# Optimization experiments

Hardware: AMD Instinct MI355X
Metric: run time of the kernel (lower is better)

The kernel has to match this reference:

```python
import jax, jax.numpy as jnp
import numpy as np

N = 100000        # nodes
E = 1600000       # edges (avg degree 16)
IN_DIM = 256      # = H * OUT_DIM so residual is active
OUT_DIM = 32
H = 8             # heads
EPS = 1e-5        # BatchNorm eps


def setup_inputs() -> dict:
    key = jax.random.key(0)
    k1, k2, k3, k4, k5 = jax.random.split(key, 5)
    h = jax.random.normal(k1, (N, IN_DIM), jnp.float32)
    # per-head Linear(in_dim, out_dim, bias=False) weights, stacked: [H, O, D]
    W = jax.random.normal(k2, (H, OUT_DIM, IN_DIM), jnp.float32) / np.sqrt(IN_DIM)
    gamma = jnp.ones((H, OUT_DIM), jnp.float32)   # BN weight per head
    beta = jnp.zeros((H, OUT_DIM), jnp.float32)   # BN bias per head
    src = jax.random.randint(k3, (E,), 0, N, jnp.int32)
    dst = jax.random.randint(k4, (E,), 0, N, jnp.int32)
    e = jax.random.normal(k5, (E, 1), jnp.float32)  # edge feats: passthrough only
    return {"h": h, "W": W, "gamma": gamma, "beta": beta,
            "src": src, "dst": dst, "e": e}


def reference(h, W, gamma, beta, src, dst, e):
    # Per-head linear projection (all heads at once): z[n,h,o]
    z = jnp.einsum('nd,hod->nho', h, W)                    # [N, H, O]
    # message_func: copy src node 'z' along edges; reduce_func: sum over in-edges
    msg = z[src]                                           # [E, H, O] gather
    agg = jax.ops.segment_sum(msg, dst, num_segments=N)    # [N, H, O] scatter-add
    # BatchNorm1d per head (training-mode batch statistics, biased variance)
    mean = jnp.mean(agg, axis=0)                           # [H, O]
    var = jnp.var(agg, axis=0)                             # [H, O]
    hn = (agg - mean) * jax.lax.rsqrt(var + EPS) * gamma + beta
    hn = jax.nn.elu(hn)
    # dropout p=0.0 / eval mode -> identity
    out = hn.reshape(N, H * OUT_DIM)                       # concat heads
    # residual (in_dim == out_dim*num_heads)
    return h + out
```

## Files before the change

### kernel.cpp

```cpp
#include <hip/hip_runtime.h>
#include <hip/hip_bf16.h>

#define NCH 256
#define DIM 256
#define BN  64
#define NBMAX 2048
#define SEG 8
#define SEG2 2
#define ECHUNK 8192
#define SCAP 4096
#define NPART 64

using f32x4  = __attribute__((ext_vector_type(4))) float;
using s16x8  = __attribute__((ext_vector_type(8))) short;
using u16x8  = __attribute__((ext_vector_type(8))) unsigned short;

__device__ __forceinline__ unsigned short f2bf(float x) {
    unsigned u = __float_as_uint(x);
    u += 0x7FFFu + ((u >> 16) & 1u);
    return (unsigned short)(u >> 16);
}
__device__ __forceinline__ float bf2f(unsigned short b) {
    return __uint_as_float(((unsigned)b) << 16);
}

__device__ __forceinline__ int block_scan256_excl(int v, int* wtmp) {
    int lane = threadIdx.x & 63, wv = threadIdx.x >> 6;
    int x = v;
#pragma unroll
    for (int d = 1; d < 64; d <<= 1) {
        int t = __shfl_up(x, d);
        if (lane >= d) x += t;
    }
    if (lane == 63) wtmp[wv] = x;
    __syncthreads();
    int wbase = 0;
#pragma unroll
    for (int w = 0; w < 4; ++w) wbase += (w < wv) ? wtmp[w] : 0;
    __syncthreads();
    return wbase + x - v;
}

__device__ __forceinline__ int block_scan1024_excl(int v, int* wtmp) {
    int lane = threadIdx.x & 63, wv = threadIdx.x >> 6;
    int x = v;
#pragma unroll
    for (int d = 1; d < 64; d <<= 1) {
        int t = __shfl_up(x, d);
        if (lane >= d) x += t;
    }
    if (lane == 63) wtmp[wv] = x;
    __syncthreads();
    int wbase = 0;
#pragma unroll
    for (int w = 0; w < 16; ++w) wbase += (w < wv) ? wtmp[w] : 0;
    __syncthreads();
    return wbase + x - v;
}

__global__ __launch_bounds__(256) void cast_w_kernel(const float* __restrict__ W,
                                                     unsigned short* __restrict__ Wb) {
    int i = blockIdx.x * 256 + threadIdx.x;
    Wb[i] = f2bf(W[i]);
}

__global__ __launch_bounds__(512, 4) void gemm_z_kernel(const float* __restrict__ h,
                                                        const unsigned short* __restrict__ Wb,
                                                        unsigned short* __restrict__ z,
                                                        int N, int ntiles) {
    __shared__ __align__(16) unsigned short lds[32768];
    int by = blockIdx.y;

    const unsigned short* wsrc = Wb + (size_t)by * 32768;
    for (int it = 0; it < 8; ++it) {
        int c = it * 512 + threadIdx.x;
        int lin = c * 16;
        int dst = lin ^ (((lin >> 9) & 7) << 4);
        *reinterpret_cast<u16x8*>((char*)lds + dst) =
            *reinterpret_cast<const u16x8*>(wsrc + c * 8);
    }
    __syncthreads();

    int wv = threadIdx.x >> 6, lane = threadIdx.x & 63;
    int lrow = lane & 15;
    int lk   = (lane >> 4) * 8;

    int ldsoff[8];
#pragma unroll
    for (int kk = 0; kk < 8; ++kk)
        ldsoff[kk] = ((lrow * 512 + kk * 64 + lk * 2) ^ ((lrow & 7) << 4));

    for (int tile = blockIdx.x; tile < ntiles; tile += gridDim.x) {
        int r0 = tile * 128 + wv * 16;
        if (r0 >= N) continue;
        int row = r0 + lrow;

        float4 cur[16];
        if (row < N) {
            const float* ap = h + (size_t)row * DIM;
#pragma unroll
            for (int kk = 0; kk < 8; ++kk) {
                cur[2 * kk]     = *reinterpret_cast<const float4*>(ap + kk * 32 + lk);
                cur[2 * kk + 1] = *reinterpret_cast<const float4*>(ap + kk * 32 + lk + 4);
            }
        } else {
#pragma unroll
            for (int i = 0; i < 16; ++i) cur[i] = float4{0.f, 0.f, 0.f, 0.f};
        }

        f32x4 acc[8];
#pragma unroll
        for (int ct = 0; ct < 8; ++ct) acc[ct] = f32x4{0.f, 0.f, 0.f, 0.f};
#pragma unroll
        for (int kk = 0; kk < 8; ++kk) {
            union { s16x8 v; __hip_bfloat162 b2[4]; } u;
            float4 f0 = cur[2 * kk], f1 = cur[2 * kk + 1];
            u.b2[0] = __float22bfloat162_rn(float2{f0.x, f0.y});
            u.b2[1] = __float22bfloat162_rn(float2{f0.z, f0.w});
            u.b2[2] = __float22bfloat162_rn(float2{f1.x, f1.y});
            u.b2[3] = __float22bfloat162_rn(float2{f1.z, f1.w});
            s16x8 a = u.v;
#pragma unroll
            for (int ct = 0; ct < 8; ++ct) {
                s16x8 b = *reinterpret_cast<const s16x8*>(
                    (const char*)lds + (ldsoff[kk] + ct * 8192));
                acc[ct] = __builtin_amdgcn_mfma_f32_16x16x32_bf16(a, b, acc[ct], 0, 0, 0);
            }
        }
        int drow = (lane >> 4) * 4;
#pragma unroll
        for (int ct = 0; ct < 8; ++ct) {
#pragma unroll
            for (int r = 0; r < 4; ++r) {
                int orow = r0 + drow + r;
                if (orow < N)
                    z[(size_t)orow * NCH + by * 128 + ct * 16 + lrow] = f2bf(acc[ct][r]);
            }
        }
    }
}

__global__ __launch_bounds__(256) void bhist_kernel(const int* __restrict__ dst,
                                                    int* __restrict__ counts, int E, int NB) {
    __shared__ int cnt[NBMAX];
    int tid = threadIdx.x;
    for (int i = tid; i < NB; i += 256) cnt[i] = 0;
    __syncthreads();
    for (int j = blockIdx.x * 256 + tid; j < E; j += gridDim.x * 256)
        atomicAdd(&cnt[dst[j] >> 6], 1);
    __syncthreads();
    for (int i = tid; i < NB; i += 256)
        if (cnt[i]) atomicAdd(&counts[i], cnt[i]);
}

__global__ __launch_bounds__(256) void bscan_kernel(const int* __restrict__ counts,
                                                    int* __restrict__ bases,
                                                    int* __restrict__ cursor, int NB) {
    __shared__ int wtmp[4];
    int tid = threadIdx.x;
    int i0 = tid * SEG;
    int tsum = 0;
#pragma unroll
    for (int k = 0; k < SEG; ++k) {
        int idx = i0 + k;
        if (idx < NB) tsum += counts[idx];
    }
    int run = block_scan256_excl(tsum, wtmp);
#pragma unroll
    for (int k = 0; k < SEG; ++k) {
        int idx = i0 + k;
        if (idx < NB) {
            bases[idx]  = run;
            cursor[idx] = run;
            run += counts[idx];
        } else if (idx == NB) {
            bases[NB] = run;
        }
    }
}

__global__ __launch_bounds__(1024) void scatter1_kernel(const int* __restrict__ src,
                                                        const int* __restrict__ dst,
                                                        int* __restrict__ cursor,
                                                        unsigned* __restrict__ pairs,
                                                        int E, int NB) {
    __shared__ int cnt[NBMAX];
    __shared__ int excl0[NBMAX];
    __shared__ int gb[NBMAX];
    __shared__ unsigned staged[ECHUNK];
    __shared__ unsigned short sbkt[ECHUNK];
    __shared__ int wtmp[16];
    int tid = threadIdx.x;
    int base = blockIdx.x * ECHUNK;
    int n = min(ECHUNK, E - base);

    for (int i = tid; i < NB; i += 1024) cnt[i] = 0;
    __syncthreads();
    for (int j = tid; j < n; j += 1024)
        atomicAdd(&cnt[dst[base + j] >> 6], 1);
    __syncthreads();

    int i0 = tid * SEG2;
    int tsum = 0;
#pragma unroll
    for (int k = 0; k < SEG2; ++k) {
        int idx = i0 + k;
        if (idx < NB) tsum += cnt[idx];
    }
    int run = block_scan1024_excl(tsum, wtmp);
#pragma unroll
    for (int k = 0; k < SEG2; ++k) {
        int idx = i0 + k;
        if (idx < NB) {
            int c = cnt[idx];
            excl0[idx] = run;
            gb[idx] = c ? atomicAdd(&cursor[idx], c) : 0;
            run += c;
        }
    }
    __syncthreads();
    for (int i = tid; i < NB; i += 1024) cnt[i] = excl0[i];
    __syncthreads();
    for (int j = tid; j < n; j += 1024) {
        int d = dst[base + j];
        int b = d >> 6;
        int slot = atomicAdd(&cnt[b], 1);
        staged[slot] = (unsigned)src[base + j] | ((unsigned)(d & 63) << 17);
        sbkt[slot]   = (unsigned short)b;
    }
    __syncthreads();
    for (int j = tid; j < n; j += 1024) {
        int b = sbkt[j];
        pairs[gb[b] + (j - excl0[b])] = staged[j];
    }
}

__global__ __launch_bounds__(256) void sortb_kernel(unsigned* __restrict__ pairs,
                                                    const int* __restrict__ bases,
                                                    int* __restrict__ rowptr,
                                                    int N, int NB, int E) {
    __shared__ unsigned raw[SCAP];
    __shared__ unsigned srt[SCAP];
    __shared__ int cnt[BN];
    __shared__ int rp[BN + 1];
    __shared__ int cur[BN];
    int bkt = blockIdx.x, tid = threadIdx.x;
    int ebeg = bases[bkt];
    int ne = min(bases[bkt + 1] - ebeg, SCAP);

    if (tid < BN) cnt[tid] = 0;
    __syncthreads();
    for (int i = tid; i < ne; i += 256) {
        unsigned e = pairs[ebeg + i];
        raw[i] = e;
        atomicAdd(&cnt[(e >> 17) & 63], 1);
    }
    __syncthreads();
    if (tid < 64) {
        int x = cnt[tid];
#pragma unroll
        for (int d = 1; d < 64; d <<= 1) {
            int t = __shfl_up(x, d);
            if (tid >= d) x += t;
        }
        rp[tid + 1] = x;
        if (tid == 0) rp[0] = 0;
    }
    __syncthreads();
    if (tid < BN) cur[tid] = rp[tid];
    int node = bkt * BN + tid;
    if (tid < BN && node < N) rowptr[node] = ebeg + rp[tid];
    if (bkt == NB - 1 && tid == 0) rowptr[N] = E;
    __syncthreads();
    for (int i = tid; i < ne; i += 256) {
        unsigned e = raw[i];
        int slot = atomicAdd(&cur[(e >> 17) & 63], 1);
        srt[slot] = e & 0x1FFFFu;
    }
    __syncthreads();
    for (int i = tid; i < ne; i += 256) pairs[ebeg + i] = srt[i];
}

template <int BF16OUT>
__global__ __launch_bounds__(256) void agg_kernel(const unsigned short* __restrict__ z,
                                                  const unsigned* __restrict__ pairs,
                                                  const int* __restrict__ rowptr,
                                                  float* __restrict__ outf,
                                                  unsigned short* __restrict__ outb,
                                                  float* __restrict__ partials,
                                                  int node0, int N) {
    __shared__ float redu[4][32][17];
    int tid = threadIdx.x;
    int wv = tid >> 6, lane = tid & 63;
    int half = lane >> 5;
    int l    = lane & 31;
    const unsigned short* zb = z + l * 8;

    float sum[8], sq[8];
#pragma unroll
    for (int j = 0; j < 8; ++j) { sum[j] = 0.f; sq[j] = 0.f; }

    for (int k = 0; k < 4; ++k) {
        int node = node0 + blockIdx.x * 16 + wv * 4 + k;
        if (node >= N) break;
        int beg = rowptr[node], end = rowptr[node + 1];

        float s[8];
#pragma unroll
        for (int j = 0; j < 8; ++j) s[j] = 0.f;

        int i = beg + half;
        for (; i + 6 < end; i += 8) {
            int n0 = pairs[i];
            int n1 = pairs[i + 2];
            int n2 = pairs[i + 4];
            int n3 = pairs[i + 6];
            u16x8 v0 = *reinterpret_cast<const u16x8*>(zb + (size_t)n0 * NCH);
            u16x8 v1 = *reinterpret_cast<const u16x8*>(zb + (size_t)n1 * NCH);
            u16x8 v2 = *reinterpret_cast<const u16x8*>(zb + (size_t)n2 * NCH);
            u16x8 v3 = *reinterpret_cast<const u16x8*>(zb + (size_t)n3 * NCH);
#pragma unroll
            for (int j = 0; j < 8; ++j)
                s[j] += (bf2f(v0[j]) + bf2f(v1[j])) + (bf2f(v2[j]) + bf2f(v3[j]));
        }
        for (; i < end; i += 2) {
            int n0 = pairs[i];
            u16x8 v0 = *reinterpret_cast<const u16x8*>(zb + (size_t)n0 * NCH);
#pragma unroll
            for (int j = 0; j < 8; ++j) s[j] += bf2f(v0[j]);
        }
#pragma unroll
        for (int j = 0; j < 8; ++j) s[j] += __shfl_xor(s[j], 32);

        if (half == 0) {
            if (BF16OUT) {
                u16x8 ob;
#pragma unroll
                for (int j = 0; j < 8; ++j) ob[j] = f2bf(s[j]);
                *reinterpret_cast<u16x8*>(outb + (size_t)node * NCH + l * 8) = ob;
            } else {
                float4 o0; o0.x = s[0]; o0.y = s[1]; o0.z = s[2]; o0.w = s[3];
                float4 o1; o1.x = s[4]; o1.y = s[5]; o1.z = s[6]; o1.w = s[7];
                float* p = outf + (size_t)node * NCH + l * 8;
                *reinterpret_cast<float4*>(p)     = o0;
                *reinterpret_cast<float4*>(p + 4) = o1;
            }
#pragma unroll
            for (int j = 0; j < 8; ++j) { sum[j] += s[j]; sq[j] += s[j] * s[j]; }
        }
    }

    if (half == 0) {
#pragma unroll
        for (int j = 0; j < 8; ++j) {
            redu[wv][l][j]     = sum[j];
            redu[wv][l][j + 8] = sq[j];
        }
    }
    __syncthreads();
    {
        int c = tid;
        int lc = c >> 3, jc = c & 7;
        float v = 0.f, q = 0.f;
#pragma unroll
        for (int w = 0; w < 4; ++w) {
            v += redu[w][lc][jc];
            q += redu[w][lc][jc + 8];
        }
        float* prow = partials + (size_t)(blockIdx.x & (NPART - 1)) * 512;
        atomicAdd(&prow[c], v);
        atomicAdd(&prow[256 + c], q);
    }
}

__global__ __launch_bounds__(256) void fscale_kernel(const float* __restrict__ partials,
                                                     const float* __restrict__ gamma,
                                                     const float* __restrict__ beta,
                                                     float* __restrict__ ss, float invN) {
    int c = threadIdx.x;
    float sum = 0.f, sq = 0.f;
    for (int r = 0; r < NPART; ++r) {
        sum += partials[(size_t)r * 512 + c];
        sq  += partials[(size_t)r * 512 + 256 + c];
    }
    float mean = sum * invN;
    float var  = sq * invN - mean * mean;
    float rs   = rsqrtf(var + 1e-5f);
    float sc   = gamma[c] * rs;
    ss[c]       = sc;
    ss[256 + c] = beta[c] - mean * sc;
}

template <int BF16IN>
__global__ __launch_bounds__(256) void final_kernel(const float* __restrict__ h,
                                                    const float* __restrict__ ss,
                                                    const float* __restrict__ aggf,
                                                    const unsigned short* __restrict__ aggb,
                                                    float* __restrict__ out, int total8) {
    int tid0 = blockIdx.x * 256 + threadIdx.x;
    int stride = gridDim.x * 256;
    int cb = (tid0 & 31) * 8;
    float sc[8], sh[8];
#pragma unroll
    for (int j = 0; j < 8; ++j) {
        sc[j] = ss[cb + j];
        sh[j] = ss[256 + cb + j];
    }
    const float LOG2E = 1.44269504088896f;
    for (int i = tid0; i < total8; i += stride) {
        float a[8];
        if (BF16IN) {
            u16x8 v = *reinterpret_cast<const u16x8*>(aggb + (size_t)i * 8);
#pragma unroll
            for (int j = 0; j < 8; ++j) a[j] = bf2f(v[j]);
        } else {
            float4 x = *reinterpret_cast<const float4*>(aggf + (size_t)i * 8);
            float4 y = *reinterpret_cast<const float4*>(aggf + (size_t)i * 8 + 4);
            a[0] = x.x; a[1] = x.y; a[2] = x.z; a[3] = x.w;
            a[4] = y.x; a[5] = y.y; a[6] = y.z; a[7] = y.w;
        }
        float4 h0 = *reinterpret_cast<const float4*>(h + (size_t)i * 8);
        float4 h1 = *reinterpret_cast<const float4*>(h + (size_t)i * 8 + 4);
        float r[8];
#pragma unroll
        for (int j = 0; j < 8; ++j) {
            float y = a[j] * sc[j] + sh[j];
            float e = __builtin_amdgcn_exp2f(y * LOG2E) - 1.0f;
            r[j] = (y > 0.f) ? y : e;
        }
        float4 o0, o1;
        o0.x = h0.x + r[0]; o0.y = h0.y + r[1]; o0.z = h0.z + r[2]; o0.w = h0.w + r[3];
        o1.x = h1.x + r[4]; o1.y = h1.y + r[5]; o1.z = h1.z + r[6]; o1.w = h1.w + r[7];
        *reinterpret_cast<float4*>(out + (size_t)i * 8)     = o0;
        *reinterpret_cast<float4*>(out + (size_t)i * 8 + 4) = o1;
    }
}

extern "C" void kernel_launch(void* const* d_in, const int* in_sizes, int n_in,
                              void* d_out, int out_size, void* d_ws, size_t ws_size,
                              hipStream_t stream) {
    const float* h     = (const float*)d_in[0];
    const float* W     = (const float*)d_in[1];
    const float* gamma = (const float*)d_in[2];
    const float* beta  = (const float*)d_in[3];
    const int*   src   = (const int*)d_in[4];
    const int*   dst   = (const int*)d_in[5];
    int N = in_sizes[0] / DIM;
    int E = in_sizes[4];
    int NB = (N + BN - 1) / BN;
    float* out = (float*)d_out;

    char* ws = (char*)d_ws;
    size_t off = 0;
    auto alloc = [&](size_t bytes) {
        size_t o = off;
        off += (bytes + 255) & ~(size_t)255;
        return o;
    };
    unsigned short* z        = (unsigned short*)(ws + alloc((size_t)N * NCH * 2));
    unsigned short* Wb       = (unsigned short*)(ws + alloc((size_t)NCH * DIM * 2));
    size_t zero_begin        = off;
    int*            counts   = (int*)(ws + alloc((size_t)NB * 4));
    float*          partials = (float*)(ws + alloc((size_t)NPART * 512 * 4));
    size_t zero_end          = off;
    int*            cursor   = (int*)(ws + alloc((size_t)NB * 4));
    int*            bases    = (int*)(ws + alloc((size_t)(NB + 1) * 4));
    int*            rowptr   = (int*)(ws + alloc((size_t)(N + 1) * 4));
    float*          ss       = (float*)(ws + alloc(512 * 4));
    unsigned*       pairs    = (unsigned*)(ws + alloc((size_t)E * 4));
    size_t aggb_off          = alloc((size_t)N * NCH * 2);
    bool bf16agg = (off <= ws_size);
    unsigned short* aggb     = (unsigned short*)(ws + aggb_off);

    hipMemsetAsync(ws + zero_begin, 0, zero_end - zero_begin, stream);

    cast_w_kernel<<<(NCH * DIM) / 256, 256, 0, stream>>>(W, Wb);

    int ntiles = (N + 127) / 128;
    int gx = (ntiles + 3) / 4;
    gemm_z_kernel<<<dim3(gx, 2), 512, 0, stream>>>(h, Wb, z, N, ntiles);

    bhist_kernel<<<256, 256, 0, stream>>>(dst, counts, E, NB);
    bscan_kernel<<<1, 256, 0, stream>>>(counts, bases, cursor, NB);
    scatter1_kernel<<<(E + ECHUNK - 1) / ECHUNK, 1024, 0, stream>>>(src, dst, cursor, pairs, E, NB);
    sortb_kernel<<<NB, 256, 0, stream>>>(pairs, bases, rowptr, N, NB, E);

    int nblk = (N + 15) / 16;
    if (bf16agg)
        agg_kernel<1><<<nblk, 256, 0, stream>>>(z, pairs, rowptr, out, aggb, partials, 0, N);
    else
        agg_kernel<0><<<nblk, 256, 0, stream>>>(z, pairs, rowptr, out, aggb, partials, 0, N);

    fscale_kernel<<<1, 256, 0, stream>>>(partials, gamma, beta, ss, 1.0f / (float)N);
    int total8 = N * (NCH / 8);
    if (bf16agg)
        final_kernel<1><<<2048, 256, 0, stream>>>(h, ss, out, aggb, out, total8);
    else
        final_kernel<0><<<2048, 256, 0, stream>>>(h, ss, out, aggb, out, total8);
}
```

Measured before the change: 282.1 us.

## Fuse destination-bucket histogram into GEMM launch as extra blocks

Merges the bucket-histogram kernel into the projection GEMM kernel by appending extra thread blocks that run the histogram while the GEMM blocks compute z. This removes one kernel launch and lets the memory-bound histogram overlap with the MFMA-heavy GEMM. In exchange, the GEMM grid is fixed at 256x2 blocks and every block now reserves an additional 8KB of LDS for the histogram array, which may reduce GEMM occupancy.

```diff
diff --git a/kernel.cpp b/kernel.cpp
--- a/kernel.cpp
+++ b/kernel.cpp
@@ -64,24 +64,45 @@
     Wb[i] = f2bf(W[i]);
 }
 
-__global__ __launch_bounds__(512, 4) void gemm_z_kernel(const float* __restrict__ h,
-                                                        const unsigned short* __restrict__ Wb,
-                                                        unsigned short* __restrict__ z,
-                                                        int N, int ntiles) {
+__global__ __launch_bounds__(512, 4) void gemm_bhist_kernel(const float* __restrict__ h,
+                                                            const unsigned short* __restrict__ Wb,
+                                                            unsigned short* __restrict__ z,
+                                                            const int* __restrict__ dst,
+                                                            int* __restrict__ counts,
+                                                            int N, int ntiles, int E, int NB,
+                                                            int gemmBlocks) {
     __shared__ __align__(16) unsigned short lds[32768];
-    int by = blockIdx.y;
+    __shared__ int hcnt[NBMAX];
+    int bid = blockIdx.x;
+    int tid = threadIdx.x;
+
+    if (bid >= gemmBlocks) {
+        int nbh = gridDim.x - gemmBlocks;
+        int hb  = bid - gemmBlocks;
+        for (int i = tid; i < NB; i += 512) hcnt[i] = 0;
+        __syncthreads();
+        for (int j = hb * 512 + tid; j < E; j += nbh * 512)
+            atomicAdd(&hcnt[dst[j] >> 6], 1);
+        __syncthreads();
+        for (int i = tid; i < NB; i += 512)
+            if (hcnt[i]) atomicAdd(&counts[i], hcnt[i]);
+        return;
+    }
+
+    int x  = bid & 255;
+    int by = bid >> 8;
 
     const unsigned short* wsrc = Wb + (size_t)by * 32768;
     for (int it = 0; it < 8; ++it) {
-        int c = it * 512 + threadIdx.x;
+        int c = it * 512 + tid;
         int lin = c * 16;
-        int dst = lin ^ (((lin >> 9) & 7) << 4);
-        *reinterpret_cast<u16x8*>((char*)lds + dst) =
+        int dstb = lin ^ (((lin >> 9) & 7) << 4);
+        *reinterpret_cast<u16x8*>((char*)lds + dstb) =
             *reinterpret_cast<const u16x8*>(wsrc + c * 8);
     }
     __syncthreads();
 
-    int wv = threadIdx.x >> 6, lane = threadIdx.x & 63;
+    int wv = tid >> 6, lane = tid & 63;
     int lrow = lane & 15;
     int lk   = (lane >> 4) * 8;
 
@@ -90,7 +111,7 @@
     for (int kk = 0; kk < 8; ++kk)
         ldsoff[kk] = ((lrow * 512 + kk * 64 + lk * 2) ^ ((lrow & 7) << 4));
 
-    for (int tile = blockIdx.x; tile < ntiles; tile += gridDim.x) {
+    for (int tile = x; tile < ntiles; tile += 256) {
         int r0 = tile * 128 + wv * 16;
         if (r0 >= N) continue;
         int row = r0 + lrow;
@@ -138,19 +159,6 @@
             }
         }
     }
-}
-
-__global__ __launch_bounds__(256) void bhist_kernel(const int* __restrict__ dst,
-                                                    int* __restrict__ counts, int E, int NB) {
-    __shared__ int cnt[NBMAX];
-    int tid = threadIdx.x;
-    for (int i = tid; i < NB; i += 256) cnt[i] = 0;
-    __syncthreads();
-    for (int j = blockIdx.x * 256 + tid; j < E; j += gridDim.x * 256)
-        atomicAdd(&cnt[dst[j] >> 6], 1);
-    __syncthreads();
-    for (int i = tid; i < NB; i += 256)
-        if (cnt[i]) atomicAdd(&counts[i], cnt[i]);
 }
 
 __global__ __launch_bounds__(256) void bscan_kernel(const int* __restrict__ counts,
@@ -477,10 +485,11 @@
     cast_w_kernel<<<(NCH * DIM) / 256, 256, 0, stream>>>(W, Wb);
 
     int ntiles = (N + 127) / 128;
-    int gx = (ntiles + 3) / 4;
-    gemm_z_kernel<<<dim3(gx, 2), 512, 0, stream>>>(h, Wb, z, N, ntiles);
-
-    bhist_kernel<<<256, 256, 0, stream>>>(dst, counts, E, NB);
+    int gemmBlocks = 512;
+    int bhistBlocks = 256;
+    gemm_bhist_kernel<<<gemmBlocks + bhistBlocks, 512, 0, stream>>>(
+        h, Wb, z, dst, counts, N, ntiles, E, NB, gemmBlocks);
+
     bscan_kernel<<<1, 256, 0, stream>>>(counts, bases, cursor, NB);
     scatter1_kernel<<<(E + ECHUNK - 1) / ECHUNK, 1024, 0, stream>>>(src, dst, cursor, pairs, E, NB);
     sortb_kernel<<<NB, 256, 0, stream>>>(pairs, bases, rowptr, N, NB, E);
```

After: 265.2 us. -6.0%, faster.
